# Kernel optimization log

Measured on AMD Instinct MI355X. Metric: run time of the kernel, lower is better.

Reference implementation:

```python
import jax, jax.numpy as jnp
import numpy as np
from jax import lax

DN = ('NCHW', 'OIHW', 'NCHW')

def conv(x, w, stride=1):
    return lax.conv_general_dilated(x, w, (stride, stride), 'SAME', dimension_numbers=DN)

def setup_inputs() -> dict:
    key = jax.random.key(0)
    ks = jax.random.split(key, 8)
    B, Cin, H, W = 16, 3, 512, 512
    Cenc, Cdec, n_heads, n_classes = 64, 64, 5, 1
    s = lambda *shape: 0.05
    return {
        'x': jax.random.normal(ks[0], (B, Cin, H, W), jnp.float32),
        'cls_id': jax.random.randint(ks[1], (B,), 0, n_heads, jnp.int32),
        'enc_w': jax.random.normal(ks[2], (Cenc, Cin, 3, 3), jnp.float32) * 0.1,
        'enc_b': jax.random.normal(ks[3], (Cenc,), jnp.float32) * 0.1,
        'dec_w': jax.random.normal(ks[4], (Cdec, Cenc, 3, 3), jnp.float32) * 0.05,
        'dec_b': jax.random.normal(ks[5], (Cdec,), jnp.float32) * 0.1,
        'head_w': jax.random.normal(ks[6], (n_heads, n_classes, Cdec, 3, 3), jnp.float32) * 0.05,
        'head_b': jax.random.normal(ks[7], (n_heads, n_classes), jnp.float32) * 0.1,
    }

def reference(x, cls_id, enc_w, enc_b, dec_w, dec_b, head_w, head_b):
    # encoder: stride-2 conv + relu -> features  [B, Cenc, H/2, W/2]
    f = jax.nn.relu(conv(x, enc_w, 2) + enc_b[None, :, None, None])
    # decoder: 3x3 conv + relu -> decoder_output [B, Cdec, H/2, W/2]
    d = jax.nn.relu(conv(f, dec_w, 1) + dec_b[None, :, None, None])
    # routing: apply segmentation_head[cls_id[b]] to sample b.
    # (gather-by-id -> per-head conv -> backsort) == per-sample gathered-kernel conv
    wk = head_w[cls_id]  # [B, n_classes, Cdec, 3, 3]
    bk = head_b[cls_id]  # [B, n_classes]
    def one_sample(di, wi):  # di: [Cdec,Hd,Wd], wi: [n_classes,Cdec,3,3]
        return conv(di[None], wi, 1)[0]
    masks = jax.vmap(one_sample)(d, wk) + bk[:, :, None, None]
    return masks  # [B, n_classes, H/2, W/2]
```

## Files before the change

### kernel.cpp

```cpp
#include <hip/hip_runtime.h>
#include <stdint.h>

#define NIMG 16
#define HIN 512
#define WIN 512
#define HO 256
#define WO 256
#define HP 258
#define WP 258

typedef unsigned short bf16_t;
typedef unsigned int u32;
typedef short bf16x8 __attribute__((ext_vector_type(8)));
typedef float f32x4 __attribute__((ext_vector_type(4)));
typedef float f32x16 __attribute__((ext_vector_type(16)));


static __device__ __forceinline__ bf16_t f2bf(float f) {
    u32 u = __float_as_uint(f);
    u += 0x7FFFu + ((u >> 16) & 1u);
    return (bf16_t)(u >> 16);
}
static __device__ __forceinline__ float bf_lo(u32 u) { return __uint_as_float(u << 16); }
static __device__ __forceinline__ float bf_hi(u32 u) { return __uint_as_float(u & 0xFFFF0000u); }
static __device__ __forceinline__ u32 pack2(float a, float b) {
    return (u32)f2bf(a) | ((u32)f2bf(b) << 16);
}

__global__ void repack_w(const float* __restrict__ dec_w, const float* __restrict__ enc_w,
                         bf16_t* __restrict__ wB, bf16_t* __restrict__ wEB) {
    int i = blockIdx.x * 256 + threadIdx.x;
    if (i < 36864) {
        int j  = i & 7;
        int l  = (i >> 3) & 63;
        int q  = (i >> 9) & 1;
        int kc = (i >> 10) & 3;
        int r  = i >> 12;
        int co  = q * 32 + (l & 31);
        int pos = kc * 16 + ((l >> 5) & 1) * 8 + j;
        int ci  = (pos & 1) * 32 + (pos >> 1);
        wB[i] = f2bf(dec_w[(co * 64 + ci) * 9 + r]);
    } else if (i < 36864 + 2048) {
        int t = i - 36864;
        int j = t & 7;
        int l = (t >> 3) & 63;
        int n = (t >> 9) & 1;
        int s = (t >> 10) & 1;
        int co = n * 32 + (l & 31);
        int k  = s * 16 + ((l >> 5) & 1) * 8 + j;
        wEB[t] = (k < 27) ? f2bf(enc_w[co * 27 + k]) : (bf16_t)0;
    }
}

__global__ void zero_halo(bf16_t* __restrict__ buf, int nimg) {
    const int per_img = 1028 * 8;
    int i = blockIdx.x * 256 + threadIdx.x;
    if (i >= nimg * per_img) return;
    int z = i / per_img;
    int rem = i - z * per_img;
    int p = rem >> 3, q = rem & 7;
    int row, col;
    if (p < 258)      { row = 0;           col = p; }
    else if (p < 516) { row = 257;         col = p - 258; }
    else if (p < 772) { row = p - 516 + 1; col = 0; }
    else              { row = p - 772 + 1; col = 257; }
    *(uint4*)(buf + ((size_t)z * HP * WP + (size_t)row * WP + col) * 64 + q * 8) =
        make_uint4(0u, 0u, 0u, 0u);
}

__global__ __launch_bounds__(512) void encoder_mfma(
    const float* __restrict__ x, const bf16_t* __restrict__ wEB,
    const float* __restrict__ enc_b, bf16_t* __restrict__ f, int b0)
{
    __shared__ __align__(16) bf16_t xt[3][33][34];

    const int tid = threadIdx.x;
    const int w   = tid >> 6;
    const int l   = tid & 63;
    const int z   = blockIdx.z;
    const int b   = b0 + z;
    const int Y0  = blockIdx.y << 5;
    const int X0  = blockIdx.x << 5;

    const int col = l & 31;
    const float bias0 = enc_b[col];
    const float bias1 = enc_b[32 + col];

    const bf16x8* wv = (const bf16x8*)wEB;
    bf16x8 Bf[2][2];
    #pragma unroll
    for (int s = 0; s < 2; ++s) {
        Bf[s][0] = wv[((s * 2 + 0) << 6) + l];
        Bf[s][1] = wv[((s * 2 + 1) << 6) + l];
    }

    const float* xb = x + (size_t)b * 3 * HIN * WIN;
    for (int i = tid; i < 3267; i += 512) {
        int ci  = i / 1089;
        int rem = i - ci * 1089;
        int yy  = rem / 33, xx = rem - yy * 33;
        int iy = Y0 + yy, ix = X0 + xx;
        float v = (iy < HIN && ix < WIN)
                ? xb[(size_t)ci * HIN * WIN + (size_t)iy * WIN + ix] : 0.f;
        xt[ci][yy][xx] = f2bf(v);
    }
    __syncthreads();

    const int row = l & 31;
    const int py  = 2 * w + (row >> 4);
    const int px  = row & 15;
    const int kh  = (l >> 5) * 8;
    bf16x8 A[2];
    #pragma unroll
    for (int s = 0; s < 2; ++s) {
        #pragma unroll
        for (int j = 0; j < 8; ++j) {
            int k = s * 16 + kh + j;
            k = k < 27 ? k : 26;
            int ci  = (k * 29) >> 8;
            int tap = k - ci * 9;
            int dy  = (tap * 11) >> 5;
            int dx  = tap - dy * 3;
            A[s][j] = (short)xt[ci][2 * py + dy][2 * px + dx];
        }
    }

    f32x16 acc[2];
    acc[0] = (f32x16){0.f,0.f,0.f,0.f,0.f,0.f,0.f,0.f,0.f,0.f,0.f,0.f,0.f,0.f,0.f,0.f};
    acc[1] = acc[0];
    acc[0] = __builtin_amdgcn_mfma_f32_32x32x16_bf16(A[0], Bf[0][0], acc[0], 0, 0, 0);
    acc[1] = __builtin_amdgcn_mfma_f32_32x32x16_bf16(A[0], Bf[0][1], acc[1], 0, 0, 0);
    acc[0] = __builtin_amdgcn_mfma_f32_32x32x16_bf16(A[1], Bf[1][0], acc[0], 0, 0, 0);
    acc[1] = __builtin_amdgcn_mfma_f32_32x32x16_bf16(A[1], Bf[1][1], acc[1], 0, 0, 0);

    bf16_t* fz = f + (size_t)z * HP * WP * 64;
    const int by = blockIdx.y << 4, bx = blockIdx.x << 4;
    #pragma unroll
    for (int v = 0; v < 16; ++v) {
        const int grow = (v & 3) + 8 * (v >> 2) + 4 * (l >> 5);
        const int flat = w * 32 + grow;
        const int pyy = flat >> 4, pxx = flat & 15;
        float t0 = acc[0][v] + bias0;  t0 = t0 > 0.f ? t0 : 0.f;
        float t1 = acc[1][v] + bias1;  t1 = t1 > 0.f ? t1 : 0.f;
        *(u32*)(fz + ((size_t)(by + pyy + 1) * WP + (bx + pxx + 1)) * 64 + 2 * col) =
            pack2(t0, t1);
    }
}

__global__ __launch_bounds__(256, 6) void decoder_mfma(
    const bf16_t* __restrict__ f, const bf16_t* __restrict__ wB,
    const float* __restrict__ dec_b, bf16_t* __restrict__ d)
{
    __shared__ __align__(16) bf16_t tile[10 * 18 * 64];

    const int tid = threadIdx.x;
    const int w   = tid >> 6;
    const int l   = tid & 63;
    const int z   = blockIdx.z;
    const int y0  = blockIdx.y << 3;
    const int x0  = blockIdx.x << 4;

    const int col = l & 31;
    const float bias0 = dec_b[col];
    const float bias1 = dec_b[32 + col];

    const bf16_t* fbase = f + ((size_t)z * HP * WP + (size_t)y0 * WP + x0) * 64;
    for (int i = tid; i < 1440; i += 256) {
        int p   = i >> 3, qq = i & 7;
        int yy  = p / 18, xx = p - yy * 18;
        uint4 v = *(const uint4*)(fbase + ((size_t)yy * WP + xx) * 64 + qq * 8);
        int byteoff = (p * 128 + qq * 16) ^ ((p & 7) << 4);
        *(uint4*)((char*)tile + byteoff) = v;
    }

    f32x16 acc[2];
    acc[0] = (f32x16){0.f,0.f,0.f,0.f,0.f,0.f,0.f,0.f,0.f,0.f,0.f,0.f,0.f,0.f,0.f,0.f};
    acc[1] = acc[0];

    __syncthreads();

    const bf16x8* wBv = (const bf16x8*)wB;
    const int ty_l = (l >> 4) & 1;
    const int tx_l = l & 15;
    const int kh16 = (l >> 5) << 4;

    #pragma unroll
    for (int r = 0; r < 9; ++r) {
        const int dy = r / 3, dx = r - 3 * (r / 3);
        bf16x8 Bf[4][2];
        #pragma unroll
        for (int kc = 0; kc < 4; ++kc) {
            Bf[kc][0] = wBv[(((r * 4 + kc) << 1) + 0) * 64 + l];
            Bf[kc][1] = wBv[(((r * 4 + kc) << 1) + 1) * 64 + l];
        }
        const int p   = (2 * w + ty_l + dy) * 18 + tx_l + dx;
        const int swz = (p & 7) << 4;
        const int pb  = p * 128 + kh16;
        #pragma unroll
        for (int kc = 0; kc < 4; ++kc) {
            bf16x8 a = *(const bf16x8*)((const char*)tile + ((pb + kc * 32) ^ swz));
            acc[0] = __builtin_amdgcn_mfma_f32_32x32x16_bf16(a, Bf[kc][0], acc[0], 0, 0, 0);
            acc[1] = __builtin_amdgcn_mfma_f32_32x32x16_bf16(a, Bf[kc][1], acc[1], 0, 0, 0);
        }
    }

    bf16_t* dz = d + (size_t)z * HP * WP * 64;
    #pragma unroll
    for (int v = 0; v < 16; ++v) {
        const int grow = (v & 3) + 8 * (v >> 2) + 4 * (l >> 5);
        const int flat = w * 32 + grow;
        const int py = flat >> 4, px = flat & 15;
        float t0 = acc[0][v] + bias0;  t0 = t0 > 0.f ? t0 : 0.f;
        float t1 = acc[1][v] + bias1;  t1 = t1 > 0.f ? t1 : 0.f;
        *(u32*)(dz + ((size_t)(y0 + py + 1) * WP + (x0 + px + 1)) * 64 + 2 * col) =
            pack2(t0, t1);
    }
}

__global__ __launch_bounds__(256, 6) void head_kernel(
    const bf16_t* __restrict__ d, const float* __restrict__ head_w,
    const float* __restrict__ head_b, const int* __restrict__ cls_id,
    float* __restrict__ out, int b0)
{
    __shared__ __align__(16) bf16_t tile[10 * 18 * 64];
    __shared__ float hw[9][64];

    const int tid = threadIdx.x;
    const int z   = blockIdx.z;
    const int b   = b0 + z;
    const int y0  = blockIdx.y << 3;
    const int x0  = blockIdx.x << 4;
    const int cls = cls_id[b];

    for (int i = tid; i < 576; i += 256) {
        int r = i >> 6, s = i & 63;
        int ci = (s & 1) * 32 + (s >> 1);
        hw[r][s] = head_w[((size_t)cls * 64 + ci) * 9 + r];
    }
    const bf16_t* dbase = d + ((size_t)z * HP * WP + (size_t)y0 * WP + x0) * 64;
    for (int i = tid; i < 1440; i += 256) {
        int p   = i >> 3, q = i & 7;
        int yy  = p / 18, xx = p - yy * 18;
        uint4 v = *(const uint4*)(dbase + ((size_t)yy * WP + xx) * 64 + q * 8);
        int byteoff = (p * 128 + q * 16) ^ ((p & 7) << 4);
        *(uint4*)((char*)tile + byteoff) = v;
    }
    __syncthreads();

    const int half = tid & 1;
    const int px   = tid >> 1;
    const int py   = px >> 4, pxx = px & 15;
    float a0 = 0.f, a1 = 0.f, a2 = 0.f, a3 = 0.f;
    #pragma unroll 1
    for (int r = 0; r < 9; ++r) {
        const int dy = r / 3, dx = r - 3 * (r / 3);
        const int p  = (py + dy) * 18 + pxx + dx;
        const int swz = (p & 7) << 4;
        const float* wr = &hw[r][0];
        #pragma unroll
        for (int qi = 0; qi < 4; ++qi) {
            const int q = 4 * half + qi;
            uint4 v = *(const uint4*)((const char*)tile + ((p * 128 + q * 16) ^ swz));
            float4 w0 = *(const float4*)(wr + q * 8);
            float4 w1 = *(const float4*)(wr + q * 8 + 4);
            a0 = fmaf(bf_lo(v.x), w0.x, fmaf(bf_hi(v.x), w0.y, a0));
            a1 = fmaf(bf_lo(v.y), w0.z, fmaf(bf_hi(v.y), w0.w, a1));
            a2 = fmaf(bf_lo(v.z), w1.x, fmaf(bf_hi(v.z), w1.y, a2));
            a3 = fmaf(bf_lo(v.w), w1.z, fmaf(bf_hi(v.w), w1.w, a3));
        }
    }
    float tot = (a0 + a1) + (a2 + a3);
    tot += __shfl_xor(tot, 1);
    if (half == 0) {
        out[(size_t)b * (HO * WO) + (size_t)(y0 + py) * WO + (x0 + pxx)] =
            head_b[cls] + tot;
    }
}

extern "C" void kernel_launch(void* const* d_in, const int* in_sizes, int n_in,
                              void* d_out, int out_size, void* d_ws, size_t ws_size,
                              hipStream_t stream) {
    const float* x      = (const float*)d_in[0];
    const int*   cls_id = (const int*)  d_in[1];
    const float* enc_w  = (const float*)d_in[2];
    const float* enc_b  = (const float*)d_in[3];
    const float* dec_w  = (const float*)d_in[4];
    const float* dec_b  = (const float*)d_in[5];
    const float* head_w = (const float*)d_in[6];
    const float* head_b = (const float*)d_in[7];
    float* out = (float*)d_out;

    const size_t WB_RESERVE = 131072;
    const size_t PER_IMG    = (size_t)HP * WP * 64 * 2;
    char* ws = (char*)d_ws;
    bf16_t* wB  = (bf16_t*)ws;
    bf16_t* wEB = (bf16_t*)(ws + 81920);

    size_t avail = (ws_size > WB_RESERVE) ? (ws_size - WB_RESERVE) : 0;
    int C = (int)(avail / (2 * PER_IMG));
    if (C < 1) C = 1;
    if (C > NIMG) C = NIMG;

    bf16_t* fbuf = (bf16_t*)(ws + WB_RESERVE);
    bf16_t* dbuf = (bf16_t*)(ws + WB_RESERVE + (size_t)C * PER_IMG);

    repack_w<<<dim3(152), 256, 0, stream>>>(dec_w, enc_w, wB, wEB);
    {
        int nthr = C * 1028 * 8;
        int nblk = (nthr + 255) / 256;
        zero_halo<<<dim3(nblk), 256, 0, stream>>>(fbuf, C);
        zero_halo<<<dim3(nblk), 256, 0, stream>>>(dbuf, C);
    }

    int n_rounds = (NIMG + C - 1) / C;
    int per = (NIMG + n_rounds - 1) / n_rounds;
    for (int b0 = 0; b0 < NIMG; b0 += per) {
        const int n = (NIMG - b0 < per) ? (NIMG - b0) : per;
        encoder_mfma<<<dim3(16, 16, n), 512, 0, stream>>>(x, wEB, enc_b, fbuf, b0);
        decoder_mfma<<<dim3(16, 32, n), 256, 0, stream>>>(fbuf, wB, dec_b, dbuf);
        head_kernel <<<dim3(16, 32, n), 256, 0, stream>>>(dbuf, head_w, head_b, cls_id, out, b0);
    }
}
```

Measured before the change: 231.9 us.

## Enlarge decoder tile to 16x16 with 4 M-fragments per wave for weight reuse

The decoder block now covers a 16x16 output tile with 128 threads (2 waves), each wave accumulating four 32-row MFMA fragments instead of one. Each weight fragment loaded from global memory is reused across four MFMAs, and the halo overhead in the shared tile shrinks relative to the outputs computed. The cost is 128 accumulator registers per lane plus more LDS per block (about 41KB), which lowers occupancy and reduces the number of blocks available for latency hiding.

```diff
diff --git a/kernel.cpp b/kernel.cpp
--- a/kernel.cpp
+++ b/kernel.cpp
@@ -147,25 +147,24 @@
     }
 }
 
-__global__ __launch_bounds__(256, 6) void decoder_mfma(
+__global__ __launch_bounds__(128) void decoder_mfma(
     const bf16_t* __restrict__ f, const bf16_t* __restrict__ wB,
     const float* __restrict__ dec_b, bf16_t* __restrict__ d)
 {
-    __shared__ __align__(16) bf16_t tile[10 * 18 * 64];
+    __shared__ __align__(16) bf16_t tile[18 * 18 * 64];
 
     const int tid = threadIdx.x;
     const int w   = tid >> 6;
     const int l   = tid & 63;
     const int z   = blockIdx.z;
-    const int y0  = blockIdx.y << 3;
-    const int x0  = blockIdx.x << 4;
+    const int y0  = blockIdx.y << 4, x0 = blockIdx.x << 4;
 
     const int col = l & 31;
     const float bias0 = dec_b[col];
     const float bias1 = dec_b[32 + col];
 
     const bf16_t* fbase = f + ((size_t)z * HP * WP + (size_t)y0 * WP + x0) * 64;
-    for (int i = tid; i < 1440; i += 256) {
+    for (int i = tid; i < 2592; i += 128) {
         int p   = i >> 3, qq = i & 7;
         int yy  = p / 18, xx = p - yy * 18;
         uint4 v = *(const uint4*)(fbase + ((size_t)yy * WP + xx) * 64 + qq * 8);
@@ -173,9 +172,13 @@
         *(uint4*)((char*)tile + byteoff) = v;
     }
 
-    f32x16 acc[2];
-    acc[0] = (f32x16){0.f,0.f,0.f,0.f,0.f,0.f,0.f,0.f,0.f,0.f,0.f,0.f,0.f,0.f,0.f,0.f};
-    acc[1] = acc[0];
+    f32x16 acc[4][2];
+    #pragma unroll
+    for (int mf = 0; mf < 4; ++mf) {
+        acc[mf][0] = (f32x16){0.f,0.f,0.f,0.f,0.f,0.f,0.f,0.f,
+                              0.f,0.f,0.f,0.f,0.f,0.f,0.f,0.f};
+        acc[mf][1] = acc[mf][0];
+    }
 
     __syncthreads();
 
@@ -193,27 +196,33 @@
             Bf[kc][0] = wBv[(((r * 4 + kc) << 1) + 0) * 64 + l];
             Bf[kc][1] = wBv[(((r * 4 + kc) << 1) + 1) * 64 + l];
         }
-        const int p   = (2 * w + ty_l + dy) * 18 + tx_l + dx;
-        const int swz = (p & 7) << 4;
-        const int pb  = p * 128 + kh16;
-        #pragma unroll
-        for (int kc = 0; kc < 4; ++kc) {
-            bf16x8 a = *(const bf16x8*)((const char*)tile + ((pb + kc * 32) ^ swz));
-            acc[0] = __builtin_amdgcn_mfma_f32_32x32x16_bf16(a, Bf[kc][0], acc[0], 0, 0, 0);
-            acc[1] = __builtin_amdgcn_mfma_f32_32x32x16_bf16(a, Bf[kc][1], acc[1], 0, 0, 0);
+        #pragma unroll
+        for (int mf = 0; mf < 4; ++mf) {
+            const int p   = (2 * (4 * w + mf) + ty_l + dy) * 18 + tx_l + dx;
+            const int swz = (p & 7) << 4;
+            const int pb  = p * 128 + kh16;
+            #pragma unroll
+            for (int kc = 0; kc < 4; ++kc) {
+                bf16x8 a = *(const bf16x8*)((const char*)tile + ((pb + kc * 32) ^ swz));
+                acc[mf][0] = __builtin_amdgcn_mfma_f32_32x32x16_bf16(a, Bf[kc][0], acc[mf][0], 0, 0, 0);
+                acc[mf][1] = __builtin_amdgcn_mfma_f32_32x32x16_bf16(a, Bf[kc][1], acc[mf][1], 0, 0, 0);
+            }
         }
     }
 
     bf16_t* dz = d + (size_t)z * HP * WP * 64;
     #pragma unroll
-    for (int v = 0; v < 16; ++v) {
-        const int grow = (v & 3) + 8 * (v >> 2) + 4 * (l >> 5);
-        const int flat = w * 32 + grow;
-        const int py = flat >> 4, px = flat & 15;
-        float t0 = acc[0][v] + bias0;  t0 = t0 > 0.f ? t0 : 0.f;
-        float t1 = acc[1][v] + bias1;  t1 = t1 > 0.f ? t1 : 0.f;
-        *(u32*)(dz + ((size_t)(y0 + py + 1) * WP + (x0 + px + 1)) * 64 + 2 * col) =
-            pack2(t0, t1);
+    for (int mf = 0; mf < 4; ++mf) {
+        #pragma unroll
+        for (int v = 0; v < 16; ++v) {
+            const int grow = (v & 3) + 8 * (v >> 2) + 4 * (l >> 5);
+            const int flat = (4 * w + mf) * 32 + grow;
+            const int py = flat >> 4, px = flat & 15;
+            float t0 = acc[mf][0][v] + bias0;  t0 = t0 > 0.f ? t0 : 0.f;
+            float t1 = acc[mf][1][v] + bias1;  t1 = t1 > 0.f ? t1 : 0.f;
+            *(u32*)(dz + ((size_t)(y0 + py + 1) * WP + (x0 + px + 1)) * 64 + 2 * col) =
+                pack2(t0, t1);
+        }
     }
 }
 
@@ -317,7 +326,7 @@
     for (int b0 = 0; b0 < NIMG; b0 += per) {
         const int n = (NIMG - b0 < per) ? (NIMG - b0) : per;
         encoder_mfma<<<dim3(16, 16, n), 512, 0, stream>>>(x, wEB, enc_b, fbuf, b0);
-        decoder_mfma<<<dim3(16, 32, n), 256, 0, stream>>>(fbuf, wB, dec_b, dbuf);
+        decoder_mfma<<<dim3(16, 16, n), 128, 0, stream>>>(fbuf, wB, dec_b, dbuf);
         head_kernel <<<dim3(16, 32, n), 256, 0, stream>>>(dbuf, head_w, head_b, cls_id, out, b0);
     }
 }
```

New measurement: 246.5 us. 1.06x slower.
